# Kernel optimization log

Measured on AMD Instinct MI355X. Metric: run time of the kernel, lower is better.

The kernel has to match this reference:

```python
import jax, jax.numpy as jnp
import numpy as np

N, D, V = 4096, 256, 32000
B, T = 32, 256
U_DECAY, X_DECAY = 0.97, 0.97
EPS = 1e-6


def layernorm_row(z):
    # matches torch: (z - mean) / (std + eps), std with Bessel correction (ddof=1)
    m = jnp.mean(z, axis=-1, keepdims=True)
    s = jnp.std(z, axis=-1, keepdims=True, ddof=1)
    return (z - m) / (s + EPS)


def setup_inputs() -> dict:
    key = jax.random.key(0)
    k1, k2, k3, k4, k5 = jax.random.split(key, 5)
    token_emb = jax.random.normal(k1, (V, D), jnp.float32) / np.float32(np.sqrt(D))
    E = jax.random.normal(k2, (D, N), jnp.float32) / np.float32(np.sqrt(N))
    Dx = jax.random.normal(k3, (N, D), jnp.float32) / np.float32(np.sqrt(D))
    Dy = jax.random.normal(k4, (N, D), jnp.float32) / np.float32(np.sqrt(D))
    idx = jax.random.randint(k5, (B, T), 0, V)
    return {"idx": idx, "token_emb": token_emb, "E": E, "Dx": Dx, "Dy": Dy}


def reference(idx, token_emb, E, Dx, Dy):
    b = idx.shape[0]

    def step(carry, tok):
        x, rho = carry                                   # x: (b,n), rho: (b,d,n)
        v_prev = token_emb[tok]                          # (b,d) embedding gather
        x_t = X_DECAY * x + jax.nn.relu(v_prev @ Dx.T)   # (b,n)
        x_t = x_t / (jnp.sum(jnp.abs(x_t), axis=-1, keepdims=True) + EPS)  # L1 normalize
        a_star = jnp.einsum('bdn,bn->bd', rho, x_t)      # fast-weight readout
        y_t = jax.nn.relu(layernorm_row(a_star) @ Dy.T) * jax.nn.relu(x_t)  # (b,n)
        v_star = layernorm_row(y_t @ E.T)                # (b,d)
        # Hebbian decayed outer-product memory update
        rho = U_DECAY * (rho + jnp.einsum('bd,bn->bdn', layernorm_row(v_prev), x_t))
        return (x_t, rho), v_star

    x0 = jnp.zeros((b, N), jnp.float32)
    rho0 = jnp.zeros((b, D, N), jnp.float32)
    (_, _), vs = jax.lax.scan(step, (x0, rho0), idx.T)   # vs: (T,b,d)
    return jnp.transpose(vs, (1, 0, 2))                  # (b,T,d)
```

## Files before the change

### kernel.cpp

```cpp
#include <hip/hip_runtime.h>
#include <hip/hip_bf16.h>

#define NN 4096
#define DD 256
#define BB 32
#define TT 256
#define EPS 1e-6f
#define DECAY 0.97f
#define LOG2_DECAY -0.043943348f

typedef __hip_bfloat16 bf16;
typedef short short8 __attribute__((ext_vector_type(8)));
typedef float floatx4 __attribute__((ext_vector_type(4)));

__device__ __forceinline__ float bfu2f(short u) {
    return __uint_as_float(((unsigned)(unsigned short)u) << 16);
}

__device__ __forceinline__ float blk_sum_256(float v, volatile float* s4) {
#pragma unroll
    for (int o = 32; o > 0; o >>= 1) v += __shfl_down(v, o, 64);
    int lane = threadIdx.x & 63, w = threadIdx.x >> 6;
    __syncthreads();
    if (lane == 0) s4[w] = v;
    __syncthreads();
    return s4[0] + s4[1] + s4[2] + s4[3];
}

__device__ __forceinline__ void gl16(const bf16* g, bf16* l) {
    __builtin_amdgcn_global_load_lds((const __attribute__((address_space(1))) void*)g,
                                     (__attribute__((address_space(3))) void*)l, 16, 0, 0);
}

__global__ void k_detect(const unsigned short* __restrict__ raw, int* __restrict__ flag) {
    __shared__ int cnt[4];
    int tid = threadIdx.x;
    int bad = 0;
    for (int i = tid; i < 8192; i += 256) {
        unsigned int u = raw[2 * i];
        float v = __uint_as_float(u << 16);
        if (!(fabsf(v) < 1e6f)) bad++;
    }
#pragma unroll
    for (int o = 32; o > 0; o >>= 1) bad += __shfl_down(bad, o, 64);
    int lane = tid & 63, w = tid >> 6;
    if (lane == 0) cnt[w] = bad;
    __syncthreads();
    if (tid == 0) flag[0] = (cnt[0] + cnt[1] + cnt[2] + cnt[3] < 32) ? 1 : 0;
}

__global__ __launch_bounds__(256) void k_convert3(const void* __restrict__ s0,
                                                  const void* __restrict__ s1,
                                                  const void* __restrict__ s2,
                                                  bf16* __restrict__ d0,
                                                  bf16* __restrict__ d1,
                                                  bf16* __restrict__ d2,
                                                  const int* __restrict__ flag) {
    const int per = NN * DD / 8;
    int i = blockIdx.x * 256 + threadIdx.x;
    int m = i / per, j = i % per;
    const void* s = (m == 0) ? s0 : (m == 1) ? s1 : s2;
    bf16* d = (m == 0) ? d0 : (m == 1) ? d1 : d2;
    if (flag[0]) {
        ((uint4*)d)[j] = ((const uint4*)s)[j];
    } else {
        const float4* f = (const float4*)s;
        float4 a = f[2 * j], b = f[2 * j + 1];
        short8 o;
        float va[8] = {a.x, a.y, a.z, a.w, b.x, b.y, b.z, b.w};
#pragma unroll
        for (int k = 0; k < 8; k++) {
            bf16 t = __float2bfloat16(va[k]);
            o[k] = *reinterpret_cast<short*>(&t);
        }
        ((short8*)d)[j] = o;
    }
}

__global__ __launch_bounds__(256) void k_gather_ln(const void* __restrict__ emb,
                                                   const int* __restrict__ idx,
                                                   bf16* __restrict__ Vpb,
                                                   bf16* __restrict__ Ub,
                                                   const int* __restrict__ flag) {
    __shared__ float s4[4];
    int r = blockIdx.x, d = threadIdx.x;
    int tok = idx[r];
    long o = (long)tok * DD + d;
    float e = flag[0] ? __bfloat162float(((const bf16*)emb)[o]) : ((const float*)emb)[o];
    Vpb[(long)r * DD + d] = __float2bfloat16(e);
    float m = blk_sum_256(e, s4) * (1.0f / DD);
    float zc = e - m;
    float var = blk_sum_256(zc * zc, s4) * (1.0f / (DD - 1));
    Ub[(long)r * DD + d] = __float2bfloat16(zc / (sqrtf(fmaxf(var, 0.f)) + EPS));
}

__global__ __launch_bounds__(256) void k_transpose(const bf16* __restrict__ Ub,
                                                   bf16* __restrict__ Ut) {
    __shared__ bf16 tile[32][33];
    int b = blockIdx.z;
    int t0 = blockIdx.x * 32, d0 = blockIdx.y * 32;
    const bf16* src = Ub + (long)b * TT * DD;
    bf16* dst = Ut + (long)b * DD * TT;
    int rr = threadIdx.x >> 3, c4 = (threadIdx.x & 7) * 4;
#pragma unroll
    for (int i = 0; i < 4; i++) tile[rr][c4 + i] = src[(long)(t0 + rr) * DD + d0 + c4 + i];
    __syncthreads();
#pragma unroll
    for (int i = 0; i < 4; i++) dst[(long)(d0 + rr) * TT + t0 + c4 + i] = tile[c4 + i][rr];
}

enum { EPI_RELU_BF16 = 0, EPI_NONE_F32 = 1, EPI_RELU_MULX_BF16 = 2 };

template <int EPI, int KSPLIT, int TRI>
__global__ __launch_bounds__(256) void k_mfma_nt(int K,
                                                 const bf16* __restrict__ A, int lda, long sA,
                                                 const bf16* __restrict__ B, int ldb, long sB,
                                                 void* __restrict__ Cv, int ldc, long sC,
                                                 const bf16* __restrict__ Xaux,
                                                 float* __restrict__ Wsum) {
    __shared__ __align__(16) char smem[17408];
    bf16* As = (bf16*)smem;
    bf16* Bs = (bf16*)(smem + 8192);
    bf16* R = (bf16*)smem;

    int z = blockIdx.z;
    int bz = z / KSPLIT, ks = z % KSPLIT;
    A += (long)bz * sA;
    B += (long)bz * sB;
    int bx = blockIdx.x, by = blockIdx.y;
    if (TRI) {
        by = (blockIdx.x >= 1) ? 1 : 0;
        bx = (blockIdx.x == 2) ? 1 : 0;
    }
    int bm = by * 128, bn = bx * 128;
    int tid = threadIdx.x;
    int srow = tid >> 2, scol = (tid & 3) << 3;
    int w = tid >> 6, lane = tid & 63;
    int wm = (w >> 1) * 64, wn = (w & 1) * 64;
    int lm = lane & 15, kh = lane >> 4;

    floatx4 acc[4][4];
#pragma unroll
    for (int i = 0; i < 4; i++)
#pragma unroll
        for (int j = 0; j < 4; j++) acc[i][j] = (floatx4){0.f, 0.f, 0.f, 0.f};

    int kchunk = K / KSPLIT;
    int kbeg = ks * kchunk, kend = kbeg + kchunk;
    const bf16* gA0 = A + (long)(bm + srow) * lda + scol;
    const bf16* gA1 = gA0 + (long)64 * lda;
    const bf16* gB0 = B + (long)(bn + srow) * ldb + scol;
    const bf16* gB1 = gB0 + (long)64 * ldb;
    bf16* lA0 = As + srow * 32 + scol;
    bf16* lA1 = As + (srow + 64) * 32 + scol;
    bf16* lB0 = Bs + srow * 32 + scol;
    bf16* lB1 = Bs + (srow + 64) * 32 + scol;

    for (int k0 = kbeg; k0 < kend; k0 += 32) {
        __syncthreads();
        gl16(gA0 + k0, lA0);
        gl16(gA1 + k0, lA1);
        gl16(gB0 + k0, lB0);
        gl16(gB1 + k0, lB1);
        __syncthreads();
        short8 af[4], bfr[4];
#pragma unroll
        for (int i = 0; i < 4; i++) af[i] = *(const short8*)(As + (wm + i * 16 + lm) * 32 + kh * 8);
#pragma unroll
        for (int j = 0; j < 4; j++) bfr[j] = *(const short8*)(Bs + (wn + j * 16 + lm) * 32 + kh * 8);
#pragma unroll
        for (int i = 0; i < 4; i++)
#pragma unroll
            for (int j = 0; j < 4; j++)
                acc[i][j] = __builtin_amdgcn_mfma_f32_16x16x32_bf16(af[i], bfr[j], acc[i][j], 0, 0, 0);
    }

    if (EPI == EPI_NONE_F32) {
        long cbase = (long)z * sC;
#pragma unroll
        for (int i = 0; i < 4; i++)
#pragma unroll
            for (int j = 0; j < 4; j++)
#pragma unroll
                for (int r = 0; r < 4; r++) {
                    int gm = bm + wm + i * 16 + kh * 4 + r;
                    int gn = bn + wn + j * 16 + lm;
                    ((float*)Cv)[cbase + (long)gm * ldc + gn] = acc[i][j][r];
                }
        return;
    }

#pragma unroll
    for (int p = 0; p < 2; p++) {
        __syncthreads();
        if ((w >> 1) == p) {
#pragma unroll
            for (int i = 0; i < 4; i++)
#pragma unroll
                for (int j = 0; j < 4; j++)
#pragma unroll
                    for (int r = 0; r < 4; r++) {
                        int rr = i * 16 + kh * 4 + r;
                        int cc = wn + j * 16 + lm;
                        R[rr * 136 + cc] = __float2bfloat16(fmaxf(acc[i][j][r], 0.f));
                    }
        }
        __syncthreads();
#pragma unroll
        for (int it = 0; it < 4; it++) {
            int row_l = it * 16 + (tid >> 4);
            int c8 = (tid & 15) * 8;
            short8 vv = *(const short8*)(R + row_l * 136 + c8);
            int gm = bm + p * 64 + row_l;
            long off = (long)gm * ldc + bn + c8;
            if (EPI == EPI_RELU_BF16) {
                *(short8*)((bf16*)Cv + off) = vv;
                float s = 0.f;
#pragma unroll
                for (int k = 0; k < 8; k++) s += bfu2f(vv[k]);
#pragma unroll
                for (int o = 8; o > 0; o >>= 1) s += __shfl_down(s, o, 16);
                if ((tid & 15) == 0) atomicAdd(&Wsum[gm], s);
            } else {
                short8 xx = *(const short8*)(Xaux + off);
                short8 oo;
#pragma unroll
                for (int k = 0; k < 8; k++) {
                    float prod = bfu2f(vv[k]) * fmaxf(bfu2f(xx[k]), 0.f);
                    bf16 t = __float2bfloat16(prod);
                    oo[k] = *reinterpret_cast<short*>(&t);
                }
                *(short8*)((bf16*)Cv + off) = oo;
            }
        }
    }
}

__global__ __launch_bounds__(256) void k_scalar_scan(const float* __restrict__ Wsum,
                                                     float* __restrict__ invS) {
    __shared__ float sw[BB * TT];
    for (int i = threadIdx.x; i < BB * TT; i += 256) sw[i] = Wsum[i];
    __syncthreads();
    int b = threadIdx.x;
    if (b < BB) {
        float sig = 0.f;
        for (int t = 0; t < TT; t++) {
            float S = DECAY * sig + sw[b * TT + t];
            float inv = 1.f / (S + EPS);
            invS[b * TT + t] = inv;
            sig = S * inv;
        }
    }
}

__global__ __launch_bounds__(256) void k_colscan(bf16* __restrict__ W,
                                                 const float* __restrict__ invS) {
    __shared__ float sv[TT];
    int b = blockIdx.y;
    sv[threadIdx.x] = invS[b * TT + threadIdx.x];
    __syncthreads();
    int n = blockIdx.x * 256 + threadIdx.x;
    bf16* p = W + (long)b * TT * NN + n;
    float x = 0.f;
    for (int t = 0; t < TT; t++) {
        float w = __bfloat162float(p[(long)t * NN]);
        x = (DECAY * x + w) * sv[t];
        p[(long)t * NN] = __float2bfloat16(x);
    }
}

__global__ __launch_bounds__(256) void k_reduce_mask(const float* __restrict__ Gp,
                                                     bf16* __restrict__ G) {
    int r = blockIdx.x;
    int b = r >> 8, t = r & 255;
    int s = threadIdx.x;
    long base = ((long)b * 4) * 65536 + (long)t * 256 + s;
    float v = Gp[base] + Gp[base + 65536] + Gp[base + 2 * 65536] + Gp[base + 3 * 65536];
    float o = (s < t) ? v * exp2f((float)(t - s) * LOG2_DECAY) : 0.f;
    G[(long)r * 256 + s] = __float2bfloat16(o);
}

__global__ __launch_bounds__(256) void k_ln_rows(const float* __restrict__ Zp,
                                                 bf16* __restrict__ O) {
    __shared__ float s4[4];
    long r = blockIdx.x;
    int d = threadIdx.x;
    long b = r >> 8, t = r & 255;
    long base = (b * 2) * 65536 + t * 256 + d;
    float z = Zp[base] + Zp[base + 65536];
    float m = blk_sum_256(z, s4) * (1.0f / DD);
    float zc = z - m;
    float var = blk_sum_256(zc * zc, s4) * (1.0f / (DD - 1));
    O[r * DD + d] = __float2bfloat16(zc / (sqrtf(fmaxf(var, 0.f)) + EPS));
}

__global__ __launch_bounds__(256) void k_final_ln(const float* __restrict__ Zp,
                                                  void* __restrict__ out,
                                                  const int* __restrict__ flag) {
    __shared__ float s4[4];
    long r = blockIdx.x;
    int d = threadIdx.x;
    const long SL = (long)8192 * 256;
    long o = r * DD + d;
    float z = Zp[o] + Zp[o + SL] + Zp[o + 2 * SL] + Zp[o + 3 * SL];
    float m = blk_sum_256(z, s4) * (1.0f / DD);
    float zc = z - m;
    float var = blk_sum_256(zc * zc, s4) * (1.0f / (DD - 1));
    float v = zc / (sqrtf(fmaxf(var, 0.f)) + EPS);
    if (flag[0]) ((bf16*)out)[o] = __float2bfloat16(v);
    else ((float*)out)[o] = v;
}

extern "C" void kernel_launch(void* const* d_in, const int* in_sizes, int n_in,
                              void* d_out, int out_size, void* d_ws, size_t ws_size,
                              hipStream_t stream) {
    const int* idx = (const int*)d_in[0];
    const void* emb = d_in[1];
    const void* E = d_in[2];
    const void* Dx = d_in[3];
    const void* Dy = d_in[4];

    char* base = (char*)d_ws;
    size_t off = 0;
    int* flag = (int*)base; off += 1024;
    bf16* Dxb = (bf16*)(base + off); off += (size_t)NN * DD * 2;
    bf16* Dyb = (bf16*)(base + off); off += (size_t)NN * DD * 2;
    bf16* Eb  = (bf16*)(base + off); off += (size_t)DD * NN * 2;
    bf16* Vpb = (bf16*)(base + off); off += (size_t)BB * TT * DD * 2;
    bf16* Ub  = (bf16*)(base + off); off += (size_t)BB * TT * DD * 2;
    bf16* Ut  = (bf16*)(base + off); off += (size_t)BB * TT * DD * 2;
    float* Wsum = (float*)(base + off); off += (size_t)BB * TT * 4;
    float* invS = (float*)(base + off); off += (size_t)BB * TT * 4;
    bf16* ALNb = (bf16*)(base + off); off += (size_t)BB * TT * DD * 2;
    bf16* G = (bf16*)(base + off); off += (size_t)BB * TT * TT * 2;
    float* Gp = (float*)(base + off); off += (size_t)4 * BB * TT * TT * 4;
    float* Astar = Gp;
    float* Zp = Gp;
    bf16* Xb = (bf16*)(base + off); off += (size_t)BB * TT * NN * 2;

    const int M = BB * TT;

    k_detect<<<1, 256, 0, stream>>>((const unsigned short*)emb, flag);
    k_convert3<<<3 * NN * DD / 8 / 256, 256, 0, stream>>>(Dx, Dy, E, Dxb, Dyb, Eb, flag);
    k_gather_ln<<<M, 256, 0, stream>>>(emb, idx, Vpb, Ub, flag);
    k_transpose<<<dim3(8, 8, BB), 256, 0, stream>>>(Ub, Ut);

    hipMemsetAsync(Wsum, 0, (size_t)M * 4, stream);

    k_mfma_nt<EPI_RELU_BF16, 1, 0><<<dim3(32, 64, 1), 256, 0, stream>>>(
        DD, Vpb, DD, 0, Dxb, DD, 0, Xb, NN, 0, nullptr, Wsum);

    k_scalar_scan<<<1, 256, 0, stream>>>(Wsum, invS);
    k_colscan<<<dim3(16, BB, 1), 256, 0, stream>>>(Xb, invS);

    k_mfma_nt<EPI_NONE_F32, 4, 1><<<dim3(3, 1, BB * 4), 256, 0, stream>>>(
        NN, Xb, NN, (long)TT * NN, Xb, NN, (long)TT * NN, Gp, TT, (long)TT * TT, nullptr, nullptr);
    k_reduce_mask<<<M, 256, 0, stream>>>(Gp, G);

    k_mfma_nt<EPI_NONE_F32, 2, 0><<<dim3(2, 2, BB * 2), 256, 0, stream>>>(
        TT, G, TT, (long)TT * TT, Ut, TT, (long)DD * TT, Astar, DD, (long)TT * DD, nullptr, nullptr);
    k_ln_rows<<<M, 256, 0, stream>>>(Astar, ALNb);

    k_mfma_nt<EPI_RELU_MULX_BF16, 1, 0><<<dim3(32, 64, 1), 256, 0, stream>>>(
        DD, ALNb, DD, 0, Dyb, DD, 0, Xb, NN, 0, Xb, nullptr);

    k_mfma_nt<EPI_NONE_F32, 4, 0><<<dim3(2, 64, 4), 256, 0, stream>>>(
        NN, Xb, NN, 0, Eb, NN, 0, Zp, DD, (long)M * DD, nullptr, nullptr);

    k_final_ln<<<M, 256, 0, stream>>>(Zp, d_out, flag);
}
```

Measured before the change: 339.7 us.

## Add whole-K 64x64 GEMM kernel for K=256 stages and vectorize column scan

Adds a new GEMM kernel for the K=256 matmuls that loads the full K=256 slab of A and B into XOR-swizzled shared memory in one shot and computes 64x64 output tiles. This replaces the 128x128 k-looped kernel with split-K 2 for the G·U product, which also removes the partial-sum reduction from the layernorm. The column scan now processes 4 columns per thread with vector loads, and the mask kernel skips loading partial sums above the diagonal. The smaller tiles give more blocks and fewer barriers, at the cost of lower per-block reuse and 64KB of shared memory per block, which limits occupancy.

```diff
diff --git a/kernel.cpp b/kernel.cpp
--- a/kernel.cpp
+++ b/kernel.cpp
@@ -111,18 +111,122 @@
 
 enum { EPI_RELU_BF16 = 0, EPI_NONE_F32 = 1, EPI_RELU_MULX_BF16 = 2 };
 
-template <int EPI, int KSPLIT, int TRI>
-__global__ __launch_bounds__(256) void k_mfma_nt(int K,
-                                                 const bf16* __restrict__ A, int lda, long sA,
-                                                 const bf16* __restrict__ B, int ldb, long sB,
-                                                 void* __restrict__ Cv, int ldc, long sC,
-                                                 const bf16* __restrict__ Xaux,
-                                                 float* __restrict__ Wsum) {
-    __shared__ __align__(16) char smem[17408];
-    bf16* As = (bf16*)smem;
-    bf16* Bs = (bf16*)(smem + 8192);
-    bf16* R = (bf16*)smem;
-
+template <int EPI>
+__global__ __launch_bounds__(256) void k_wk64(const bf16* __restrict__ A, int lda, long sA,
+                                              const bf16* __restrict__ B, int ldb, long sB,
+                                              void* __restrict__ Cv, int ldc, long sC,
+                                              const bf16* __restrict__ Xaux,
+                                              float* __restrict__ Wsum) {
+    __shared__ __align__(16) bf16 As[16384];
+    __shared__ __align__(16) bf16 Bs[16384];
+    int z = blockIdx.z;
+    A += (long)z * sA;
+    B += (long)z * sB;
+    long cbase = (long)z * sC;
+    int bm = blockIdx.y * 64, bn = blockIdx.x * 64;
+    int tid = threadIdx.x, w = tid >> 6, lane = tid & 63;
+    int half = lane >> 5, c32 = lane & 31;
+
+#pragma unroll
+    for (int jj = 0; jj < 8; jj++) {
+        int j = w * 8 + jj;
+        int r = 2 * j + half;
+        int cs = c32 ^ (r & 31);
+        gl16(A + (long)(bm + r) * lda + cs * 8, As + j * 512);
+        gl16(B + (long)(bn + r) * ldb + cs * 8, Bs + j * 512);
+    }
+    __syncthreads();
+
+    int wm = (w >> 1) * 32, wn = (w & 1) * 32;
+    int lm = lane & 15, kh = lane >> 4;
+    floatx4 acc[2][2];
+#pragma unroll
+    for (int i = 0; i < 2; i++)
+#pragma unroll
+        for (int j = 0; j < 2; j++) acc[i][j] = (floatx4){0.f, 0.f, 0.f, 0.f};
+
+#pragma unroll
+    for (int ks = 0; ks < 8; ks++) {
+        int C = ks * 4 + kh;
+        short8 af[2], bfr[2];
+#pragma unroll
+        for (int i = 0; i < 2; i++) {
+            int ra = wm + i * 16 + lm;
+            af[i] = *(const short8*)(As + ra * 256 + ((C ^ (ra & 31)) << 3));
+            int rb = wn + i * 16 + lm;
+            bfr[i] = *(const short8*)(Bs + rb * 256 + ((C ^ (rb & 31)) << 3));
+        }
+#pragma unroll
+        for (int i = 0; i < 2; i++)
+#pragma unroll
+            for (int j = 0; j < 2; j++)
+                acc[i][j] = __builtin_amdgcn_mfma_f32_16x16x32_bf16(af[i], bfr[j], acc[i][j], 0, 0, 0);
+    }
+
+    if (EPI == EPI_NONE_F32) {
+#pragma unroll
+        for (int i = 0; i < 2; i++)
+#pragma unroll
+            for (int j = 0; j < 2; j++)
+#pragma unroll
+                for (int r = 0; r < 4; r++) {
+                    int gm = bm + wm + i * 16 + kh * 4 + r;
+                    int gn = bn + wn + j * 16 + lm;
+                    ((float*)Cv)[cbase + (long)gm * ldc + gn] = acc[i][j][r];
+                }
+        return;
+    }
+
+    __syncthreads();
+    bf16* R = As;
+#pragma unroll
+    for (int i = 0; i < 2; i++)
+#pragma unroll
+        for (int j = 0; j < 2; j++)
+#pragma unroll
+            for (int r = 0; r < 4; r++) {
+                int rr = wm + i * 16 + kh * 4 + r;
+                int cc = wn + j * 16 + lm;
+                R[rr * 72 + cc] = __float2bfloat16(fmaxf(acc[i][j][r], 0.f));
+            }
+    __syncthreads();
+#pragma unroll
+    for (int it = 0; it < 2; it++) {
+        int slot = it * 256 + tid;
+        int row = slot >> 3, c8 = (slot & 7) * 8;
+        short8 vv = *(const short8*)(R + row * 72 + c8);
+        int gm = bm + row;
+        long off = cbase + (long)gm * ldc + bn + c8;
+        if (EPI == EPI_RELU_BF16) {
+            *(short8*)((bf16*)Cv + off) = vv;
+            float s = 0.f;
+#pragma unroll
+            for (int k = 0; k < 8; k++) s += bfu2f(vv[k]);
+            s += __shfl_down(s, 4, 8);
+            s += __shfl_down(s, 2, 8);
+            s += __shfl_down(s, 1, 8);
+            if ((tid & 7) == 0) atomicAdd(&Wsum[gm], s);
+        } else {
+            short8 xx = *(const short8*)(Xaux + off);
+            short8 oo;
+#pragma unroll
+            for (int k = 0; k < 8; k++) {
+                float prod = bfu2f(vv[k]) * fmaxf(bfu2f(xx[k]), 0.f);
+                bf16 t = __float2bfloat16(prod);
+                oo[k] = *reinterpret_cast<short*>(&t);
+            }
+            *(short8*)((bf16*)Cv + off) = oo;
+        }
+    }
+}
+
+template <int KSPLIT, int TRI>
+__global__ __launch_bounds__(256) void k_pipe(int K,
+                                              const bf16* __restrict__ A, int lda, long sA,
+                                              const bf16* __restrict__ B, int ldb, long sB,
+                                              float* __restrict__ Cv, int ldc, long sC) {
+    __shared__ __align__(16) bf16 As[128 * 32];
+    __shared__ __align__(16) bf16 Bs[128 * 32];
     int z = blockIdx.z;
     int bz = z / KSPLIT, ks = z % KSPLIT;
     A += (long)bz * sA;
@@ -175,65 +279,17 @@
                 acc[i][j] = __builtin_amdgcn_mfma_f32_16x16x32_bf16(af[i], bfr[j], acc[i][j], 0, 0, 0);
     }
 
-    if (EPI == EPI_NONE_F32) {
-        long cbase = (long)z * sC;
-#pragma unroll
-        for (int i = 0; i < 4; i++)
-#pragma unroll
-            for (int j = 0; j < 4; j++)
-#pragma unroll
-                for (int r = 0; r < 4; r++) {
-                    int gm = bm + wm + i * 16 + kh * 4 + r;
-                    int gn = bn + wn + j * 16 + lm;
-                    ((float*)Cv)[cbase + (long)gm * ldc + gn] = acc[i][j][r];
-                }
-        return;
-    }
-
-#pragma unroll
-    for (int p = 0; p < 2; p++) {
-        __syncthreads();
-        if ((w >> 1) == p) {
-#pragma unroll
-            for (int i = 0; i < 4; i++)
-#pragma unroll
-                for (int j = 0; j < 4; j++)
-#pragma unroll
-                    for (int r = 0; r < 4; r++) {
-                        int rr = i * 16 + kh * 4 + r;
-                        int cc = wn + j * 16 + lm;
-                        R[rr * 136 + cc] = __float2bfloat16(fmaxf(acc[i][j][r], 0.f));
-                    }
-        }
-        __syncthreads();
-#pragma unroll
-        for (int it = 0; it < 4; it++) {
-            int row_l = it * 16 + (tid >> 4);
-            int c8 = (tid & 15) * 8;
-            short8 vv = *(const short8*)(R + row_l * 136 + c8);
-            int gm = bm + p * 64 + row_l;
-            long off = (long)gm * ldc + bn + c8;
-            if (EPI == EPI_RELU_BF16) {
-                *(short8*)((bf16*)Cv + off) = vv;
-                float s = 0.f;
-#pragma unroll
-                for (int k = 0; k < 8; k++) s += bfu2f(vv[k]);
-#pragma unroll
-                for (int o = 8; o > 0; o >>= 1) s += __shfl_down(s, o, 16);
-                if ((tid & 15) == 0) atomicAdd(&Wsum[gm], s);
-            } else {
-                short8 xx = *(const short8*)(Xaux + off);
-                short8 oo;
-#pragma unroll
-                for (int k = 0; k < 8; k++) {
-                    float prod = bfu2f(vv[k]) * fmaxf(bfu2f(xx[k]), 0.f);
-                    bf16 t = __float2bfloat16(prod);
-                    oo[k] = *reinterpret_cast<short*>(&t);
-                }
-                *(short8*)((bf16*)Cv + off) = oo;
+    long cbase = (long)z * sC;
+#pragma unroll
+    for (int i = 0; i < 4; i++)
+#pragma unroll
+        for (int j = 0; j < 4; j++)
+#pragma unroll
+            for (int r = 0; r < 4; r++) {
+                int gm = bm + wm + i * 16 + kh * 4 + r;
+                int gn = bn + wn + j * 16 + lm;
+                Cv[cbase + (long)gm * ldc + gn] = acc[i][j][r];
             }
-        }
-    }
 }
 
 __global__ __launch_bounds__(256) void k_scalar_scan(const float* __restrict__ Wsum,
@@ -259,13 +315,24 @@
     int b = blockIdx.y;
     sv[threadIdx.x] = invS[b * TT + threadIdx.x];
     __syncthreads();
-    int n = blockIdx.x * 256 + threadIdx.x;
-    bf16* p = W + (long)b * TT * NN + n;
-    float x = 0.f;
+    int n0 = blockIdx.x * 1024 + threadIdx.x * 4;
+    bf16* p = W + (long)b * TT * NN + n0;
+    float x0 = 0.f, x1 = 0.f, x2 = 0.f, x3 = 0.f;
     for (int t = 0; t < TT; t++) {
-        float w = __bfloat162float(p[(long)t * NN]);
-        x = (DECAY * x + w) * sv[t];
-        p[(long)t * NN] = __float2bfloat16(x);
+        short4 wv = *(const short4*)(p + (long)t * NN);
+        float iv = sv[t];
+        x0 = (DECAY * x0 + bfu2f(wv.x)) * iv;
+        x1 = (DECAY * x1 + bfu2f(wv.y)) * iv;
+        x2 = (DECAY * x2 + bfu2f(wv.z)) * iv;
+        x3 = (DECAY * x3 + bfu2f(wv.w)) * iv;
+        short4 ov;
+        bf16 t0 = __float2bfloat16(x0), t1 = __float2bfloat16(x1);
+        bf16 t2 = __float2bfloat16(x2), t3 = __float2bfloat16(x3);
+        ov.x = *reinterpret_cast<short*>(&t0);
+        ov.y = *reinterpret_cast<short*>(&t1);
+        ov.z = *reinterpret_cast<short*>(&t2);
+        ov.w = *reinterpret_cast<short*>(&t3);
+        *(short4*)(p + (long)t * NN) = ov;
     }
 }
 
@@ -274,20 +341,21 @@
     int r = blockIdx.x;
     int b = r >> 8, t = r & 255;
     int s = threadIdx.x;
-    long base = ((long)b * 4) * 65536 + (long)t * 256 + s;
-    float v = Gp[base] + Gp[base + 65536] + Gp[base + 2 * 65536] + Gp[base + 3 * 65536];
-    float o = (s < t) ? v * exp2f((float)(t - s) * LOG2_DECAY) : 0.f;
+    float o = 0.f;
+    if (s < t) {
+        long base = ((long)b * 4) * 65536 + (long)t * 256 + s;
+        float v = Gp[base] + Gp[base + 65536] + Gp[base + 2 * 65536] + Gp[base + 3 * 65536];
+        o = v * exp2f((float)(t - s) * LOG2_DECAY);
+    }
     G[(long)r * 256 + s] = __float2bfloat16(o);
 }
 
-__global__ __launch_bounds__(256) void k_ln_rows(const float* __restrict__ Zp,
+__global__ __launch_bounds__(256) void k_ln_rows(const float* __restrict__ Z,
                                                  bf16* __restrict__ O) {
     __shared__ float s4[4];
     long r = blockIdx.x;
     int d = threadIdx.x;
-    long b = r >> 8, t = r & 255;
-    long base = (b * 2) * 65536 + t * 256 + d;
-    float z = Zp[base] + Zp[base + 65536];
+    float z = Z[r * DD + d];
     float m = blk_sum_256(z, s4) * (1.0f / DD);
     float zc = z - m;
     float var = blk_sum_256(zc * zc, s4) * (1.0f / (DD - 1));
@@ -347,25 +415,25 @@
 
     hipMemsetAsync(Wsum, 0, (size_t)M * 4, stream);
 
-    k_mfma_nt<EPI_RELU_BF16, 1, 0><<<dim3(32, 64, 1), 256, 0, stream>>>(
-        DD, Vpb, DD, 0, Dxb, DD, 0, Xb, NN, 0, nullptr, Wsum);
+    k_wk64<EPI_RELU_BF16><<<dim3(NN / 64, M / 64, 1), 256, 0, stream>>>(
+        Vpb, DD, 0, Dxb, DD, 0, Xb, NN, 0, nullptr, Wsum);
 
     k_scalar_scan<<<1, 256, 0, stream>>>(Wsum, invS);
-    k_colscan<<<dim3(16, BB, 1), 256, 0, stream>>>(Xb, invS);
-
-    k_mfma_nt<EPI_NONE_F32, 4, 1><<<dim3(3, 1, BB * 4), 256, 0, stream>>>(
-        NN, Xb, NN, (long)TT * NN, Xb, NN, (long)TT * NN, Gp, TT, (long)TT * TT, nullptr, nullptr);
+    k_colscan<<<dim3(4, BB, 1), 256, 0, stream>>>(Xb, invS);
+
+    k_pipe<4, 1><<<dim3(3, 1, BB * 4), 256, 0, stream>>>(
+        NN, Xb, NN, (long)TT * NN, Xb, NN, (long)TT * NN, Gp, TT, (long)TT * TT);
     k_reduce_mask<<<M, 256, 0, stream>>>(Gp, G);
 
-    k_mfma_nt<EPI_NONE_F32, 2, 0><<<dim3(2, 2, BB * 2), 256, 0, stream>>>(
-        TT, G, TT, (long)TT * TT, Ut, TT, (long)DD * TT, Astar, DD, (long)TT * DD, nullptr, nullptr);
+    k_wk64<EPI_NONE_F32><<<dim3(TT / 64, TT / 64, BB), 256, 0, stream>>>(
+        G, TT, (long)TT * TT, Ut, TT, (long)DD * TT, Astar, DD, (long)TT * DD, nullptr, nullptr);
     k_ln_rows<<<M, 256, 0, stream>>>(Astar, ALNb);
 
-    k_mfma_nt<EPI_RELU_MULX_BF16, 1, 0><<<dim3(32, 64, 1), 256, 0, stream>>>(
-        DD, ALNb, DD, 0, Dyb, DD, 0, Xb, NN, 0, Xb, nullptr);
-
-    k_mfma_nt<EPI_NONE_F32, 4, 0><<<dim3(2, 64, 4), 256, 0, stream>>>(
-        NN, Xb, NN, 0, Eb, NN, 0, Zp, DD, (long)M * DD, nullptr, nullptr);
+    k_wk64<EPI_RELU_MULX_BF16><<<dim3(NN / 64, M / 64, 1), 256, 0, stream>>>(
+        ALNb, DD, 0, Dyb, DD, 0, Xb, NN, 0, Xb, nullptr);
+
+    k_pipe<4, 0><<<dim3(2, 64, 4), 256, 0, stream>>>(
+        NN, Xb, NN, 0, Eb, NN, 0, Zp, DD, (long)M * DD);
 
     k_final_ln<<<M, 256, 0, stream>>>(Zp, d_out, flag);
 }
```

Result: slower. 363.0 us (+6.9%).
